# Kernel optimization log

Hardware: AMD Instinct MI355X
Metric: run time of the kernel (lower is better)

The kernel has to match this reference:

```python
import jax, jax.numpy as jnp
import numpy as np
from jax import lax

KERNEL = 3
STRIDE = 2
PADDING = 1


def setup_inputs() -> dict:
    key = jax.random.key(0)
    x = jax.random.normal(key, (32, 64, 224, 224), dtype=jnp.float32)
    return {"x": x}


def reference(x) -> jnp.ndarray:
    # Torch semantics: pad with -inf first, then take max over each k x k window.
    neg_inf = jnp.asarray(-jnp.inf, dtype=x.dtype)
    if PADDING > 0:
        x = jnp.pad(
            x,
            ((0, 0), (0, 0), (PADDING, PADDING), (PADDING, PADDING)),
            constant_values=-jnp.inf,
        )
    # Windowed max over spatial dims only (N, C untouched).
    out = lax.reduce_window(
        x,
        neg_inf,
        lax.max,
        window_dimensions=(1, 1, KERNEL, KERNEL),
        window_strides=(1, 1, STRIDE, STRIDE),
        padding="VALID",
    )
    return out
```

## Files before the change

### kernel.cpp

```cpp
#include <hip/hip_runtime.h>
#include <math.h>


#define IH 224
#define IW 224
#define OH 112
#define OW 112
#define OW_GROUPS 28

__global__ void maxpool2d_k3s2p1_kernel(const float* __restrict__ in,
                                        float* __restrict__ out,
                                        int total_groups) {
    int idx = blockIdx.x * blockDim.x + threadIdx.x;
    if (idx >= total_groups) return;

    int g    = idx % OW_GROUPS;
    int rest = idx / OW_GROUPS;
    int oh   = rest % OH;
    int nc   = rest / OH;

    const float* base = in + (size_t)nc * (IH * IW);
    const int iw0 = g * 8;
    const int ih_start = 2 * oh - 1;

    float m0 = -INFINITY, m1 = -INFINITY, m2 = -INFINITY, m3 = -INFINITY;

    #pragma unroll
    for (int r = 0; r < 3; ++r) {
        int ih = ih_start + r;
        if (ih < 0) continue;
        const float* rp = base + (size_t)ih * IW + iw0;
        float4 a = *reinterpret_cast<const float4*>(rp);
        float4 b = *reinterpret_cast<const float4*>(rp + 4);
        float left = (g == 0) ? -INFINITY : rp[-1];

        m0 = fmaxf(m0, fmaxf(left, fmaxf(a.x, a.y)));
        m1 = fmaxf(m1, fmaxf(a.y,  fmaxf(a.z, a.w)));
        m2 = fmaxf(m2, fmaxf(a.w,  fmaxf(b.x, b.y)));
        m3 = fmaxf(m3, fmaxf(b.y,  fmaxf(b.z, b.w)));
    }

    float4 o = make_float4(m0, m1, m2, m3);
    float* op = out + ((size_t)(nc * OH + oh) * OW) + g * 4;
    *reinterpret_cast<float4*>(op) = o;
}

extern "C" void kernel_launch(void* const* d_in, const int* in_sizes, int n_in,
                              void* d_out, int out_size, void* d_ws, size_t ws_size,
                              hipStream_t stream) {
    (void)in_sizes; (void)n_in; (void)d_ws; (void)ws_size; (void)out_size;
    const float* x = (const float*)d_in[0];
    float* out = (float*)d_out;

    const int NC = 32 * 64;
    const int total_groups = NC * OH * OW_GROUPS;
    const int block = 256;
    const int grid = (total_groups + block - 1) / block;

    maxpool2d_k3s2p1_kernel<<<grid, block, 0, stream>>>(x, out, total_groups);
}
```

Baseline: 99.23 us.

## Compute four output rows per thread to reuse overlapping input rows

Each thread now covers a tile of four output rows instead of one. It loads nine input rows once and accumulates each row's horizontal max into every output row whose window includes it. This removes the redundant re-reads of shared boundary rows, going from twelve row loads to nine per four outputs, and stores with nontemporal hints. In exchange there are four times fewer threads, more registers per thread, and less parallelism to hide memory latency.

```diff
diff --git a/kernel.cpp b/kernel.cpp
--- a/kernel.cpp
+++ b/kernel.cpp
@@ -7,42 +7,66 @@
 #define OH 112
 #define OW 112
 #define OW_GROUPS 28
+#define OH_TILES  28
+
+typedef float f32x4 __attribute__((ext_vector_type(4)));
 
 __global__ void maxpool2d_k3s2p1_kernel(const float* __restrict__ in,
                                         float* __restrict__ out,
-                                        int total_groups) {
+                                        int total_tiles) {
     int idx = blockIdx.x * blockDim.x + threadIdx.x;
-    if (idx >= total_groups) return;
+    if (idx >= total_tiles) return;
 
     int g    = idx % OW_GROUPS;
     int rest = idx / OW_GROUPS;
-    int oh   = rest % OH;
-    int nc   = rest / OH;
+    int t    = rest % OH_TILES;
+    int nc   = rest / OH_TILES;
 
     const float* base = in + (size_t)nc * (IH * IW);
-    const int iw0 = g * 8;
-    const int ih_start = 2 * oh - 1;
+    const int iw0     = g * 8;
+    const int ihbase  = t * 8;
 
-    float m0 = -INFINITY, m1 = -INFINITY, m2 = -INFINITY, m3 = -INFINITY;
+    float m[4][4];
+    #pragma unroll
+    for (int lo = 0; lo < 4; ++lo)
+        #pragma unroll
+        for (int j = 0; j < 4; ++j)
+            m[lo][j] = -INFINITY;
 
     #pragma unroll
-    for (int r = 0; r < 3; ++r) {
-        int ih = ih_start + r;
-        if (ih < 0) continue;
+    for (int s = -1; s <= 7; ++s) {
+        int ih = ihbase + s;
+        if (s == -1 && ih < 0) continue;
+
         const float* rp = base + (size_t)ih * IW + iw0;
-        float4 a = *reinterpret_cast<const float4*>(rp);
-        float4 b = *reinterpret_cast<const float4*>(rp + 4);
+        f32x4 a = *reinterpret_cast<const f32x4*>(rp);
+        f32x4 b = *reinterpret_cast<const f32x4*>(rp + 4);
         float left = (g == 0) ? -INFINITY : rp[-1];
 
-        m0 = fmaxf(m0, fmaxf(left, fmaxf(a.x, a.y)));
-        m1 = fmaxf(m1, fmaxf(a.y,  fmaxf(a.z, a.w)));
-        m2 = fmaxf(m2, fmaxf(a.w,  fmaxf(b.x, b.y)));
-        m3 = fmaxf(m3, fmaxf(b.y,  fmaxf(b.z, b.w)));
+        float h0 = fmaxf(left, fmaxf(a.x, a.y));
+        float h1 = fmaxf(a.y,  fmaxf(a.z, a.w));
+        float h2 = fmaxf(a.w,  fmaxf(b.x, b.y));
+        float h3 = fmaxf(b.y,  fmaxf(b.z, b.w));
+
+        #pragma unroll
+        for (int lo = 0; lo < 4; ++lo) {
+            if (s >= 2 * lo - 1 && s <= 2 * lo + 1) {
+                m[lo][0] = fmaxf(m[lo][0], h0);
+                m[lo][1] = fmaxf(m[lo][1], h1);
+                m[lo][2] = fmaxf(m[lo][2], h2);
+                m[lo][3] = fmaxf(m[lo][3], h3);
+            }
+        }
     }
 
-    float4 o = make_float4(m0, m1, m2, m3);
-    float* op = out + ((size_t)(nc * OH + oh) * OW) + g * 4;
-    *reinterpret_cast<float4*>(op) = o;
+    #pragma unroll
+    for (int lo = 0; lo < 4; ++lo) {
+        int oh = t * 4 + lo;
+        f32x4 o;
+        o.x = m[lo][0]; o.y = m[lo][1]; o.z = m[lo][2]; o.w = m[lo][3];
+        float* op = out + ((size_t)(nc * OH + oh) * OW) + g * 4;
+        __builtin_nontemporal_store(o, reinterpret_cast<f32x4*>(op));
+    }
 }
 
 extern "C" void kernel_launch(void* const* d_in, const int* in_sizes, int n_in,
@@ -53,9 +77,9 @@
     float* out = (float*)d_out;
 
     const int NC = 32 * 64;
-    const int total_groups = NC * OH * OW_GROUPS;
+    const int total_tiles = NC * OH_TILES * OW_GROUPS;
     const int block = 256;
-    const int grid = (total_groups + block - 1) / block;
+    const int grid = (total_tiles + block - 1) / block;
 
-    maxpool2d_k3s2p1_kernel<<<grid, block, 0, stream>>>(x, out, total_groups);
+    maxpool2d_k3s2p1_kernel<<<grid, block, 0, stream>>>(x, out, total_tiles);
 }
```

After: 88.67 us (median of 2 runs). -10.6%, faster.

## Stage 33-row input bands in LDS and compute 16 output rows per block

Applied to the files above, without the earlier changes.

Each block now loads a band of 33 input rows of one channel into shared memory, then 224 threads compute 16 output rows from LDS. The global reads that were repeated for rows shared between adjacent output rows are replaced by a single coalesced load plus LDS reuse. Output stores are made nontemporal. The cost is about 29.5 KB of LDS per block, which may limit occupancy, a __syncthreads barrier with no overlap of load and compute, and 32 of 256 threads idle during compute.

```diff
diff --git a/kernel.cpp b/kernel.cpp
--- a/kernel.cpp
+++ b/kernel.cpp
@@ -6,43 +6,71 @@
 #define IW 224
 #define OH 112
 #define OW 112
-#define OW_GROUPS 28
+#define BAND_OUT 16
+#define BAND_IN  33
+#define NBANDS   7
+#define VEC_PER_ROW 56
+#define STAGE_VECS (BAND_IN * VEC_PER_ROW)
+
+typedef float f32x4 __attribute__((ext_vector_type(4)));
 
 __global__ void maxpool2d_k3s2p1_kernel(const float* __restrict__ in,
-                                        float* __restrict__ out,
-                                        int total_groups) {
-    int idx = blockIdx.x * blockDim.x + threadIdx.x;
-    if (idx >= total_groups) return;
+                                        float* __restrict__ out) {
+    __shared__ __align__(16) float smem[BAND_IN * IW];
 
-    int g    = idx % OW_GROUPS;
-    int rest = idx / OW_GROUPS;
-    int oh   = rest % OH;
-    int nc   = rest / OH;
+    const int band = blockIdx.x % NBANDS;
+    const int nc   = blockIdx.x / NBANDS;
+    const int tid  = threadIdx.x;
 
     const float* base = in + (size_t)nc * (IH * IW);
-    const int iw0 = g * 8;
-    const int ih_start = 2 * oh - 1;
-
-    float m0 = -INFINITY, m1 = -INFINITY, m2 = -INFINITY, m3 = -INFINITY;
+    const int gi0 = 32 * band - 1;
 
     #pragma unroll
-    for (int r = 0; r < 3; ++r) {
-        int ih = ih_start + r;
-        if (ih < 0) continue;
-        const float* rp = base + (size_t)ih * IW + iw0;
-        float4 a = *reinterpret_cast<const float4*>(rp);
-        float4 b = *reinterpret_cast<const float4*>(rp + 4);
-        float left = (g == 0) ? -INFINITY : rp[-1];
-
-        m0 = fmaxf(m0, fmaxf(left, fmaxf(a.x, a.y)));
-        m1 = fmaxf(m1, fmaxf(a.y,  fmaxf(a.z, a.w)));
-        m2 = fmaxf(m2, fmaxf(a.w,  fmaxf(b.x, b.y)));
-        m3 = fmaxf(m3, fmaxf(b.y,  fmaxf(b.z, b.w)));
+    for (int i = tid; i < STAGE_VECS; i += 256) {
+        int li = i / VEC_PER_ROW;
+        int ci = i % VEC_PER_ROW;
+        int gi = gi0 + li;
+        f32x4 v;
+        if (gi >= 0) {
+            v = *reinterpret_cast<const f32x4*>(base + (size_t)gi * IW + ci * 4);
+        } else {
+            v.x = v.y = v.z = v.w = -INFINITY;
+        }
+        *reinterpret_cast<f32x4*>(&smem[li * IW + ci * 4]) = v;
     }
 
-    float4 o = make_float4(m0, m1, m2, m3);
-    float* op = out + ((size_t)(nc * OH + oh) * OW) + g * 4;
-    *reinterpret_cast<float4*>(op) = o;
+    __syncthreads();
+
+    if (tid < 224) {
+        const int g  = tid % 28;
+        const int rr = tid / 28;
+
+        #pragma unroll
+        for (int q = 0; q < 2; ++q) {
+            const int ro = 2 * rr + q;
+            float m0 = -INFINITY, m1 = -INFINITY, m2 = -INFINITY, m3 = -INFINITY;
+
+            #pragma unroll
+            for (int k = 0; k < 3; ++k) {
+                const int li = 2 * ro + k;
+                const float* rp = &smem[li * IW + g * 8];
+                f32x4 a = *reinterpret_cast<const f32x4*>(rp);
+                f32x4 b = *reinterpret_cast<const f32x4*>(rp + 4);
+                float left = (g == 0) ? -INFINITY : rp[-1];
+
+                m0 = fmaxf(m0, fmaxf(left, fmaxf(a.x, a.y)));
+                m1 = fmaxf(m1, fmaxf(a.y,  fmaxf(a.z, a.w)));
+                m2 = fmaxf(m2, fmaxf(a.w,  fmaxf(b.x, b.y)));
+                m3 = fmaxf(m3, fmaxf(b.y,  fmaxf(b.z, b.w)));
+            }
+
+            const int oh = band * BAND_OUT + ro;
+            f32x4 o;
+            o.x = m0; o.y = m1; o.z = m2; o.w = m3;
+            float* op = out + ((size_t)(nc * OH + oh) * OW) + g * 4;
+            __builtin_nontemporal_store(o, reinterpret_cast<f32x4*>(op));
+        }
+    }
 }
 
 extern "C" void kernel_launch(void* const* d_in, const int* in_sizes, int n_in,
@@ -53,9 +81,6 @@
     float* out = (float*)d_out;
 
     const int NC = 32 * 64;
-    const int total_groups = NC * OH * OW_GROUPS;
-    const int block = 256;
-    const int grid = (total_groups + block - 1) / block;
-
-    maxpool2d_k3s2p1_kernel<<<grid, block, 0, stream>>>(x, out, total_groups);
+    const int grid = NC * NBANDS;
+    maxpool2d_k3s2p1_kernel<<<grid, 256, 0, stream>>>(x, out);
 }
```

New measurement: 94.42 us. -4.8%, faster.
